# Performance work log

Measured on AMD Instinct MI355X. Metric: run time of the kernel, lower is better.

Reference implementation:

```python
import jax, jax.numpy as jnp
import numpy as np

# model hyperparameters (from init_kwargs 'model' mapping)
SIG = 10.0       # kernel length scale
C = 0.0          # energy integration constant
STD = 1.0        # normalization std
M, N_ATOMS = 64, 24
T_ROWS, DESC = 6000, N_ATOMS * (N_ATOMS - 1) // 2  # 276


def setup_inputs() -> dict:
    key = jax.random.key(0)
    k1, k2, k3 = jax.random.split(key, 3)
    # spread atoms out so pairwise distances are O(1..10) Angstrom-like
    Rs = jax.random.normal(k1, (M, N_ATOMS, 3), jnp.float32) * 3.0
    # training descriptors are inverse distances -> positive values in (0,1)
    xs_train = jax.random.uniform(k2, (T_ROWS, DESC), jnp.float32)
    Jx_alphas = jax.random.normal(k3, (T_ROWS, DESC), jnp.float32) * 0.1
    return {"Rs": Rs, "xs_train": xs_train, "Jx_alphas": Jx_alphas}


def reference(Rs, xs_train, Jx_alphas):
    sig = SIG
    q = np.sqrt(5.0) / sig
    m, n = Rs.shape[0], Rs.shape[1]
    i, j = np.tril_indices(n, k=-1)  # lower-triangular atom pairs, P entries

    # pairwise coordinate differences [M, N, N, 3]
    diffs = Rs[:, :, None, :] - Rs[:, None, :, :]
    # inverse pairwise distances over tril pairs -> descriptor xs [M, P]
    d_ij = jnp.linalg.norm(diffs[:, i, j, :], axis=-1)
    xs = 1.0 / d_ij

    # descriptor differences to all (permuted) training points [M, T, P]
    x_diffs = q * xs[:, None, :] - q * xs_train[None, :, :]
    x_dists = jnp.linalg.norm(x_diffs, axis=-1)            # [M, T]
    exp_xs = (5.0 / (3.0 * sig ** 2)) * jnp.exp(-x_dists)  # [M, T]
    dot = jnp.einsum('mtp,tp->mt', x_diffs, Jx_alphas)     # [M, T]
    exp1 = exp_xs * (1.0 + x_dists)                        # [M, T]

    F1 = jnp.einsum('mt,mtp->mp', exp_xs * dot, x_diffs)   # [M, P]
    F2 = exp1 @ Jx_alphas                                  # [M, P]
    Fs_x = (F1 - F2) * xs ** 3                             # [M, P]

    # scatter pair forces back onto the symmetric [N, N] pair grid;
    # diagonal diffs are zero so leaving mult=0 there matches the original
    mult = jnp.zeros((m, n, n), Rs.dtype)
    mult = mult.at[:, i, j].set(Fs_x).at[:, j, i].set(Fs_x)
    Fs = (diffs * mult[..., None]).sum(axis=1) * STD       # [M, N, 3]

    Es = (exp1 * dot).sum(axis=-1) / q * STD + C           # [M]
    return Es, Fs
```

## Files before the change

kernel.cpp:

```cpp
#include <hip/hip_runtime.h>
#include <math.h>

#define MM 64
#define NA 24
#define NP 276
#define NT 6000
#define NTP 6048
#define QC 0.22360679774997896f
#define EXPC 0.01666666666666667f

#define OFF_XST  0
#define OFF_UU   17664
#define OFF_ES   17728
#define OFF_SW   17792
#define OFF_SH   17856
#define OFF_WT   300480
#define OFF_ET   687552
#define ZTOT     282752

__device__ __forceinline__ float f4c(const float4& v, int i) {
  return i == 0 ? v.x : i == 1 ? v.y : i == 2 ? v.z : v.w;
}

__global__ __launch_bounds__(256) void k_pre(const float* __restrict__ Rs,
                                             float* __restrict__ ws) {
  const int tid = threadIdx.x;
  for (int z = blockIdx.x * 256 + tid; z < ZTOT; z += gridDim.x * 256)
    ws[OFF_ES + z] = 0.f;
  for (int z = blockIdx.x * 256 + tid; z < 6144; z += gridDim.x * 256) {
    if (z < 3072) ws[OFF_WT + 384000 + z] = 0.f;
    else          ws[OFF_ET + 384000 + (z - 3072)] = 0.f;
  }
  if (blockIdx.x < MM) {
    const int m = blockIdx.x;
    __shared__ float sR[NA * 3];
    __shared__ float sAcc[4];
    if (tid < NA * 3) sR[tid] = Rs[m * NA * 3 + tid];
    __syncthreads();
    float acc = 0.f;
    for (int p = tid; p < NP; p += 256) {
      int i = (int)((1.0f + sqrtf(1.0f + 8.0f * (float)p)) * 0.5f);
      while (i * (i - 1) / 2 > p) i--;
      while ((i + 1) * i / 2 <= p) i++;
      int j = p - i * (i - 1) / 2;
      float dx = sR[i * 3 + 0] - sR[j * 3 + 0];
      float dy = sR[i * 3 + 1] - sR[j * 3 + 1];
      float dz = sR[i * 3 + 2] - sR[j * 3 + 2];
      float u = 1.0f / sqrtf(dx * dx + dy * dy + dz * dz);
      ws[OFF_XST + p * 64 + m] = u;
      acc += u * u;
    }
    for (int off = 32; off; off >>= 1) acc += __shfl_down(acc, off);
    if ((tid & 63) == 0) sAcc[tid >> 6] = acc;
    __syncthreads();
    if (tid == 0) ws[OFF_UU + m] = sAcc[0] + sAcc[1] + sAcc[2] + sAcc[3];
  }
}

#define G1_BS 280
#define G1_AS 36
__global__ __launch_bounds__(256, 2) void k_g1(const float* __restrict__ xt,
                                               const float* __restrict__ Ja,
                                               float* __restrict__ ws) {
  __shared__ __align__(16) float2 Bs[16][G1_BS];
  __shared__ __align__(16) float As[NP][G1_AS];
  __shared__ float sVV[16], sC1[16];
  __shared__ float sEsW[4][32], sSwW[4][32];
  const int tid = threadIdx.x;
  const int t0 = blockIdx.x * 16;
  const int m0 = blockIdx.y * 32;

  for (int idx = tid; idx < 16 * 69; idx += 256) {
    const int row = idx / 69;
    const int kq = (idx - row * 69) * 4;
    const float4 v = *(const float4*)(xt + (size_t)(t0 + row) * NP + kq);
    const float4 j = *(const float4*)(Ja + (size_t)(t0 + row) * NP + kq);
    *(float4*)&Bs[row][kq]     = make_float4(v.x, j.x, v.y, j.y);
    *(float4*)&Bs[row][kq + 2] = make_float4(v.z, j.z, v.w, j.w);
  }
  for (int idx = tid; idx < NP * 8; idx += 256) {
    const int p = idx >> 3;
    const int mq = (idx & 7) * 4;
    *(float4*)&As[p][mq] = *(const float4*)(ws + OFF_XST + p * 64 + m0 + mq);
  }
  const int r = tid & 15;
  const int c = tid >> 4;
  const float2 uu2 = *(const float2*)(ws + OFF_UU + m0 + 2 * r);
  __syncthreads();

  {
    const int tl = tid >> 4;
    const int l16 = tid & 15;
    float a = 0.f, b = 0.f;
    for (int k = l16; k < NP; k += 16) {
      const float2 x = Bs[tl][k];
      a = fmaf(x.x, x.x, a);
      b = fmaf(x.x, x.y, b);
    }
#pragma unroll
    for (int off = 8; off; off >>= 1) {
      a += __shfl_down(a, off, 16);
      b += __shfl_down(b, off, 16);
    }
    if (l16 == 0) { sVV[tl] = a; sC1[tl] = b; }
  }
  __syncthreads();

  float av0 = 0.f, av1 = 0.f, aj0 = 0.f, aj1 = 0.f;
#pragma unroll 4
  for (int kk = 0; kk < NP; kk += 2) {
    const float4 b  = *(const float4*)&Bs[c][kk];
    const float2 a0 = *(const float2*)&As[kk][2 * r];
    const float2 a1 = *(const float2*)&As[kk + 1][2 * r];
    av0 = fmaf(a0.x, b.x, av0); aj0 = fmaf(a0.x, b.y, aj0);
    av1 = fmaf(a0.y, b.x, av1); aj1 = fmaf(a0.y, b.y, aj1);
    av0 = fmaf(a1.x, b.z, av0); aj0 = fmaf(a1.x, b.w, aj0);
    av1 = fmaf(a1.y, b.z, av1); aj1 = fmaf(a1.y, b.w, aj1);
  }

  const float vvt = sVV[c];
  const float c1t = sC1[c];
  float es2[2], sw2[2], wv[2], ev[2];
#pragma unroll
  for (int i = 0; i < 2; i++) {
    const float g1v = i ? av1 : av0;
    const float g2v = i ? aj1 : aj0;
    const float uum = i ? uu2.y : uu2.x;
    float d2 = fmaxf(uum - 2.f * g1v + vvt, 0.f);
    float xd = QC * sqrtf(d2);
    float dv = QC * (g2v - c1t);
    float ex = EXPC * __expf(-xd);
    float e1v = ex * (1.f + xd);
    float w_ = ex * dv;
    wv[i] = w_; ev[i] = e1v;
    es2[i] = e1v * dv;
    sw2[i] = w_;
  }
  const int t = t0 + c;
  *(float2*)(ws + OFF_WT + (size_t)t * 64 + m0 + 2 * r) = make_float2(wv[0], wv[1]);
  *(float2*)(ws + OFF_ET + (size_t)t * 64 + m0 + 2 * r) = make_float2(ev[0], ev[1]);

#pragma unroll
  for (int i = 0; i < 2; i++) {
    es2[i] += __shfl_down(es2[i], 32); es2[i] += __shfl_down(es2[i], 16);
    sw2[i] += __shfl_down(sw2[i], 32); sw2[i] += __shfl_down(sw2[i], 16);
  }
  const int w = tid >> 6;
  if ((tid & 63) < 16) {
    sEsW[w][2 * r + 0] = es2[0]; sEsW[w][2 * r + 1] = es2[1];
    sSwW[w][2 * r + 0] = sw2[0]; sSwW[w][2 * r + 1] = sw2[1];
  }
  __syncthreads();
  if (tid < 32) {
    const float es = sEsW[0][tid] + sEsW[1][tid] + sEsW[2][tid] + sEsW[3][tid];
    const float sw = sSwW[0][tid] + sSwW[1][tid] + sSwW[2][tid] + sSwW[3][tid];
    atomicAdd(ws + OFF_ES + m0 + tid, es);
    atomicAdd(ws + OFF_SW + m0 + tid, sw);
  }
}

#define G2_KC 96
#define G2_AS 68
#define G2_BS 18
__global__ __launch_bounds__(256, 2) void k_g2(const float* __restrict__ xt,
                                               const float* __restrict__ Ja,
                                               float* __restrict__ ws) {
  __shared__ __align__(16) float Aw[G2_KC][G2_AS];
  __shared__ __align__(16) float Ae[G2_KC][G2_AS];
  __shared__ __align__(16) float2 Bvj[G2_KC][G2_BS];
  const int tid = threadIdx.x;
  const int p0 = blockIdx.x * 16;
  const int k0 = blockIdx.y * G2_KC;
  const int validp = (NP - p0 < 16) ? (NP - p0) : 16;

  for (int idx = tid; idx < G2_KC * 16; idx += 256) {
    const int k = idx >> 4;
    const int mq = (idx & 15) * 4;
    *(float4*)&Aw[k][mq] = *(const float4*)(ws + OFF_WT + (size_t)(k0 + k) * 64 + mq);
    *(float4*)&Ae[k][mq] = *(const float4*)(ws + OFF_ET + (size_t)(k0 + k) * 64 + mq);
  }
  for (int idx = tid; idx < G2_KC * 4; idx += 256) {
    const int k = idx >> 2;
    const int pq = (idx & 3) * 4;
    const int t = k0 + k;
    float4 v = make_float4(0.f, 0.f, 0.f, 0.f), j = v;
    if (pq < validp && t < NT) {
      v = *(const float4*)(xt + (size_t)t * NP + p0 + pq);
      j = *(const float4*)(Ja + (size_t)t * NP + p0 + pq);
    }
    *(float4*)&Bvj[k][pq]     = make_float4(v.x, j.x, v.y, j.y);
    *(float4*)&Bvj[k][pq + 2] = make_float4(v.z, j.z, v.w, j.w);
  }
  __syncthreads();

  const int r = tid & 31;
  const int c = tid >> 5;
  float f1[2][2] = {{0.f, 0.f}, {0.f, 0.f}};
  float f2[2][2] = {{0.f, 0.f}, {0.f, 0.f}};
#pragma unroll 4
  for (int k = 0; k < G2_KC; k++) {
    const float2 aw = *(const float2*)&Aw[k][2 * r];
    const float2 ae = *(const float2*)&Ae[k][2 * r];
    const float4 b  = *(const float4*)&Bvj[k][2 * c];
    f1[0][0] = fmaf(aw.x, b.x, f1[0][0]); f1[0][1] = fmaf(aw.x, b.z, f1[0][1]);
    f1[1][0] = fmaf(aw.y, b.x, f1[1][0]); f1[1][1] = fmaf(aw.y, b.z, f1[1][1]);
    f2[0][0] = fmaf(ae.x, b.y, f2[0][0]); f2[0][1] = fmaf(ae.x, b.w, f2[0][1]);
    f2[1][0] = fmaf(ae.y, b.y, f2[1][0]); f2[1][1] = fmaf(ae.y, b.w, f2[1][1]);
  }

  const int sh = blockIdx.y & 7;
  float* b1 = ws + OFF_SH + (size_t)(sh * 2 + 0) * NP * 64;
  float* b2 = ws + OFF_SH + (size_t)(sh * 2 + 1) * NP * 64;
#pragma unroll
  for (int j = 0; j < 2; j++) {
    const int pl = 2 * c + j;
    if (pl < validp) {
      const int p = p0 + pl;
#pragma unroll
      for (int i = 0; i < 2; i++) {
        atomicAdd(b1 + (size_t)p * 64 + 2 * r + i, f1[i][j]);
        atomicAdd(b2 + (size_t)p * 64 + 2 * r + i, f2[i][j]);
      }
    }
  }
}

__global__ __launch_bounds__(320) void k_final(const float* __restrict__ Rs,
                                               const float* __restrict__ ws,
                                               float* __restrict__ out) {
  const int m = blockIdx.x;
  const int tid = threadIdx.x;
  __shared__ float fx[NP];
  __shared__ float sR[NA * 3];
  if (tid < NA * 3) sR[tid] = Rs[m * NA * 3 + tid];
  const float sw = ws[OFF_SW + m];
  for (int p = tid; p < NP; p += 320) {
    float f1p = 0.f, f2 = 0.f;
#pragma unroll
    for (int s = 0; s < 8; s++) {
      f1p += ws[OFF_SH + ((size_t)(s * 2 + 0) * NP + p) * 64 + m];
      f2  += ws[OFF_SH + ((size_t)(s * 2 + 1) * NP + p) * 64 + m];
    }
    const float u = ws[OFF_XST + p * 64 + m];
    const float F1 = QC * (u * sw - f1p);
    fx[p] = (F1 - f2) * u * u * u;
  }
  __syncthreads();
  if (tid == 0) out[m] = ws[OFF_ES + m] / QC;
  if (tid < NA * 3) {
    const int a = tid / 3, cc = tid % 3;
    const float ra = sR[a * 3 + cc];
    float acc = 0.f;
    for (int b = 0; b < NA; b++) {
      if (b == a) continue;
      const int i = a > b ? a : b, j = a > b ? b : a;
      const int p = i * (i - 1) / 2 + j;
      acc += (sR[b * 3 + cc] - ra) * fx[p];
    }
    out[MM + m * NA * 3 + tid] = acc;
  }
}

extern "C" void kernel_launch(void* const* d_in, const int* in_sizes, int n_in,
                              void* d_out, int out_size, void* d_ws, size_t ws_size,
                              hipStream_t stream) {
  const float* Rs = (const float*)d_in[0];
  const float* xt = (const float*)d_in[1];
  const float* Ja = (const float*)d_in[2];
  float* out = (float*)d_out;
  float* ws = (float*)d_ws;

  k_pre<<<256, 256, 0, stream>>>(Rs, ws);
  k_g1<<<dim3(375, 2), 256, 0, stream>>>(xt, Ja, ws);
  k_g2<<<dim3(18, 63), 256, 0, stream>>>(xt, Ja, ws);
  k_final<<<MM, 320, 0, stream>>>(Rs, ws, out);
}
```

Baseline: 136.2 us.

## Use split-K register tiling with shared-memory reduction in both GEMM kernels

Result: slower. 151.3 us (+11.1%).

```diff
diff --git a/kernel.cpp b/kernel.cpp
--- a/kernel.cpp
+++ b/kernel.cpp
@@ -57,18 +57,21 @@
   }
 }
 
-#define G1_BS 280
-#define G1_AS 36
+#define G1_BS 278
 __global__ __launch_bounds__(256, 2) void k_g1(const float* __restrict__ xt,
                                                const float* __restrict__ Ja,
                                                float* __restrict__ ws) {
   __shared__ __align__(16) float2 Bs[16][G1_BS];
-  __shared__ __align__(16) float As[NP][G1_AS];
+  __shared__ __align__(16) float As[NP][36];
   __shared__ float sVV[16], sC1[16];
-  __shared__ float sEsW[4][32], sSwW[4][32];
+  __shared__ __align__(16) float sRed[4][64][4];
   const int tid = threadIdx.x;
   const int t0 = blockIdx.x * 16;
   const int m0 = blockIdx.y * 32;
+  const int lane = tid & 63;
+  const int ks = tid >> 6;
+  const int mg = lane & 7;
+  const int tg = lane >> 3;
 
   for (int idx = tid; idx < 16 * 69; idx += 256) {
     const int row = idx / 69;
@@ -83,9 +86,7 @@
     const int mq = (idx & 7) * 4;
     *(float4*)&As[p][mq] = *(const float4*)(ws + OFF_XST + p * 64 + m0 + mq);
   }
-  const int r = tid & 15;
-  const int c = tid >> 4;
-  const float2 uu2 = *(const float2*)(ws + OFF_UU + m0 + 2 * r);
+  const float4 uu4 = *(const float4*)(ws + OFF_UU + m0 + mg * 4);
   __syncthreads();
 
   {
@@ -106,72 +107,109 @@
   }
   __syncthreads();
 
-  float av0 = 0.f, av1 = 0.f, aj0 = 0.f, aj1 = 0.f;
-#pragma unroll 4
-  for (int kk = 0; kk < NP; kk += 2) {
-    const float4 b  = *(const float4*)&Bs[c][kk];
-    const float2 a0 = *(const float2*)&As[kk][2 * r];
-    const float2 a1 = *(const float2*)&As[kk + 1][2 * r];
-    av0 = fmaf(a0.x, b.x, av0); aj0 = fmaf(a0.x, b.y, aj0);
-    av1 = fmaf(a0.y, b.x, av1); aj1 = fmaf(a0.y, b.y, aj1);
-    av0 = fmaf(a1.x, b.z, av0); aj0 = fmaf(a1.x, b.w, aj0);
-    av1 = fmaf(a1.y, b.z, av1); aj1 = fmaf(a1.y, b.w, aj1);
-  }
-
-  const float vvt = sVV[c];
-  const float c1t = sC1[c];
-  float es2[2], sw2[2], wv[2], ev[2];
-#pragma unroll
-  for (int i = 0; i < 2; i++) {
-    const float g1v = i ? av1 : av0;
-    const float g2v = i ? aj1 : aj0;
-    const float uum = i ? uu2.y : uu2.x;
-    float d2 = fmaxf(uum - 2.f * g1v + vvt, 0.f);
-    float xd = QC * sqrtf(d2);
-    float dv = QC * (g2v - c1t);
-    float ex = EXPC * __expf(-xd);
-    float e1v = ex * (1.f + xd);
-    float w_ = ex * dv;
-    wv[i] = w_; ev[i] = e1v;
-    es2[i] = e1v * dv;
-    sw2[i] = w_;
-  }
-  const int t = t0 + c;
-  *(float2*)(ws + OFF_WT + (size_t)t * 64 + m0 + 2 * r) = make_float2(wv[0], wv[1]);
-  *(float2*)(ws + OFF_ET + (size_t)t * 64 + m0 + 2 * r) = make_float2(ev[0], ev[1]);
-
-#pragma unroll
-  for (int i = 0; i < 2; i++) {
-    es2[i] += __shfl_down(es2[i], 32); es2[i] += __shfl_down(es2[i], 16);
-    sw2[i] += __shfl_down(sw2[i], 32); sw2[i] += __shfl_down(sw2[i], 16);
-  }
-  const int w = tid >> 6;
-  if ((tid & 63) < 16) {
-    sEsW[w][2 * r + 0] = es2[0]; sEsW[w][2 * r + 1] = es2[1];
-    sSwW[w][2 * r + 0] = sw2[0]; sSwW[w][2 * r + 1] = sw2[1];
-  }
-  __syncthreads();
-  if (tid < 32) {
-    const float es = sEsW[0][tid] + sEsW[1][tid] + sEsW[2][tid] + sEsW[3][tid];
-    const float sw = sSwW[0][tid] + sSwW[1][tid] + sSwW[2][tid] + sSwW[3][tid];
-    atomicAdd(ws + OFF_ES + m0 + tid, es);
-    atomicAdd(ws + OFF_SW + m0 + tid, sw);
+  float accv[2][4] = {{0.f,0.f,0.f,0.f},{0.f,0.f,0.f,0.f}};
+  float accj[2][4] = {{0.f,0.f,0.f,0.f},{0.f,0.f,0.f,0.f}};
+  const int kbeg = 70 * ks;
+  const int kend = (ks == 3) ? NP : kbeg + 70;
+#pragma unroll 5
+  for (int k = kbeg; k < kend; k += 2) {
+    const float4 bA = *(const float4*)&Bs[2 * tg][k];
+    const float4 bB = *(const float4*)&Bs[2 * tg + 1][k];
+    const float4 a0 = *(const float4*)&As[k][mg * 4];
+    const float4 a1 = *(const float4*)&As[k + 1][mg * 4];
+#pragma unroll
+    for (int i = 0; i < 4; i++) {
+      const float x0 = f4c(a0, i), x1 = f4c(a1, i);
+      accv[0][i] = fmaf(x0, bA.x, accv[0][i]); accj[0][i] = fmaf(x0, bA.y, accj[0][i]);
+      accv[0][i] = fmaf(x1, bA.z, accv[0][i]); accj[0][i] = fmaf(x1, bA.w, accj[0][i]);
+      accv[1][i] = fmaf(x0, bB.x, accv[1][i]); accj[1][i] = fmaf(x0, bB.y, accj[1][i]);
+      accv[1][i] = fmaf(x1, bB.z, accv[1][i]); accj[1][i] = fmaf(x1, bB.w, accj[1][i]);
+    }
+  }
+
+#pragma unroll
+  for (int ps = 0; ps < 4; ps++) {
+    __syncthreads();
+    float4 v;
+    if (ps == 0) v = make_float4(accv[0][0], accv[0][1], accv[0][2], accv[0][3]);
+    else if (ps == 1) v = make_float4(accv[1][0], accv[1][1], accv[1][2], accv[1][3]);
+    else if (ps == 2) v = make_float4(accj[0][0], accj[0][1], accj[0][2], accj[0][3]);
+    else v = make_float4(accj[1][0], accj[1][1], accj[1][2], accj[1][3]);
+    *(float4*)&sRed[ks][lane][0] = v;
+    __syncthreads();
+    if (ks == 0) {
+      const float4 s0 = *(const float4*)&sRed[0][lane][0];
+      const float4 s1 = *(const float4*)&sRed[1][lane][0];
+      const float4 s2 = *(const float4*)&sRed[2][lane][0];
+      const float4 s3 = *(const float4*)&sRed[3][lane][0];
+      const float4 s = make_float4(s0.x + s1.x + s2.x + s3.x, s0.y + s1.y + s2.y + s3.y,
+                                   s0.z + s1.z + s2.z + s3.z, s0.w + s1.w + s2.w + s3.w);
+      if (ps == 0)      { accv[0][0]=s.x; accv[0][1]=s.y; accv[0][2]=s.z; accv[0][3]=s.w; }
+      else if (ps == 1) { accv[1][0]=s.x; accv[1][1]=s.y; accv[1][2]=s.z; accv[1][3]=s.w; }
+      else if (ps == 2) { accj[0][0]=s.x; accj[0][1]=s.y; accj[0][2]=s.z; accj[0][3]=s.w; }
+      else              { accj[1][0]=s.x; accj[1][1]=s.y; accj[1][2]=s.z; accj[1][3]=s.w; }
+    }
+  }
+
+  if (ks == 0) {
+    float es4[4] = {0.f,0.f,0.f,0.f}, sw4[4] = {0.f,0.f,0.f,0.f};
+#pragma unroll
+    for (int tt = 0; tt < 2; tt++) {
+      const int t = t0 + tg * 2 + tt;
+      const float vvt = sVV[tg * 2 + tt];
+      const float c1t = sC1[tg * 2 + tt];
+      float wq[4], eq[4];
+#pragma unroll
+      for (int i = 0; i < 4; i++) {
+        float d2 = fmaxf(f4c(uu4, i) - 2.f * accv[tt][i] + vvt, 0.f);
+        float xd = QC * sqrtf(d2);
+        float dv = QC * (accj[tt][i] - c1t);
+        float ex = EXPC * __expf(-xd);
+        float e1v = ex * (1.f + xd);
+        float w_ = ex * dv;
+        wq[i] = w_; eq[i] = e1v;
+        es4[i] += e1v * dv;
+        sw4[i] += w_;
+      }
+      *(float4*)(ws + OFF_WT + (size_t)t * 64 + m0 + mg * 4) =
+          make_float4(wq[0], wq[1], wq[2], wq[3]);
+      *(float4*)(ws + OFF_ET + (size_t)t * 64 + m0 + mg * 4) =
+          make_float4(eq[0], eq[1], eq[2], eq[3]);
+    }
+#pragma unroll
+    for (int off = 8; off <= 32; off <<= 1) {
+#pragma unroll
+      for (int i = 0; i < 4; i++) {
+        es4[i] += __shfl_down(es4[i], off);
+        sw4[i] += __shfl_down(sw4[i], off);
+      }
+    }
+    if (tg == 0) {
+#pragma unroll
+      for (int i = 0; i < 4; i++) {
+        atomicAdd(ws + OFF_ES + m0 + mg * 4 + i, es4[i]);
+        atomicAdd(ws + OFF_SW + m0 + mg * 4 + i, sw4[i]);
+      }
+    }
   }
 }
 
 #define G2_KC 96
-#define G2_AS 68
-#define G2_BS 18
 __global__ __launch_bounds__(256, 2) void k_g2(const float* __restrict__ xt,
                                                const float* __restrict__ Ja,
                                                float* __restrict__ ws) {
-  __shared__ __align__(16) float Aw[G2_KC][G2_AS];
-  __shared__ __align__(16) float Ae[G2_KC][G2_AS];
-  __shared__ __align__(16) float2 Bvj[G2_KC][G2_BS];
+  __shared__ __align__(16) float Aw[G2_KC][68];
+  __shared__ __align__(16) float Ae[G2_KC][68];
+  __shared__ __align__(16) float2 Bvj[G2_KC][18];
+  __shared__ __align__(16) float sRed[4][64][8];
   const int tid = threadIdx.x;
   const int p0 = blockIdx.x * 16;
   const int k0 = blockIdx.y * G2_KC;
   const int validp = (NP - p0 < 16) ? (NP - p0) : 16;
+  const int lane = tid & 63;
+  const int ks = tid >> 6;
+  const int mg = lane & 15;
+  const int pg = lane >> 4;
 
   for (int idx = tid; idx < G2_KC * 16; idx += 256) {
     const int k = idx >> 4;
@@ -193,34 +231,72 @@
   }
   __syncthreads();
 
-  const int r = tid & 31;
-  const int c = tid >> 5;
-  float f1[2][2] = {{0.f, 0.f}, {0.f, 0.f}};
-  float f2[2][2] = {{0.f, 0.f}, {0.f, 0.f}};
+  float f1[4][4] = {{0}}, f2[4][4] = {{0}};
+  const int kb = ks * 24;
 #pragma unroll 4
-  for (int k = 0; k < G2_KC; k++) {
-    const float2 aw = *(const float2*)&Aw[k][2 * r];
-    const float2 ae = *(const float2*)&Ae[k][2 * r];
-    const float4 b  = *(const float4*)&Bvj[k][2 * c];
-    f1[0][0] = fmaf(aw.x, b.x, f1[0][0]); f1[0][1] = fmaf(aw.x, b.z, f1[0][1]);
-    f1[1][0] = fmaf(aw.y, b.x, f1[1][0]); f1[1][1] = fmaf(aw.y, b.z, f1[1][1]);
-    f2[0][0] = fmaf(ae.x, b.y, f2[0][0]); f2[0][1] = fmaf(ae.x, b.w, f2[0][1]);
-    f2[1][0] = fmaf(ae.y, b.y, f2[1][0]); f2[1][1] = fmaf(ae.y, b.w, f2[1][1]);
-  }
-
+  for (int k = kb; k < kb + 24; k++) {
+    const float4 aw = *(const float4*)&Aw[k][mg * 4];
+    const float4 ae = *(const float4*)&Ae[k][mg * 4];
+    const float4 b0 = *(const float4*)&Bvj[k][pg * 4];
+    const float4 b1 = *(const float4*)&Bvj[k][pg * 4 + 2];
+#pragma unroll
+    for (int i = 0; i < 4; i++) {
+      const float w_ = f4c(aw, i), e_ = f4c(ae, i);
+      f1[i][0] = fmaf(w_, b0.x, f1[i][0]); f2[i][0] = fmaf(e_, b0.y, f2[i][0]);
+      f1[i][1] = fmaf(w_, b0.z, f1[i][1]); f2[i][1] = fmaf(e_, b0.w, f2[i][1]);
+      f1[i][2] = fmaf(w_, b1.x, f1[i][2]); f2[i][2] = fmaf(e_, b1.y, f2[i][2]);
+      f1[i][3] = fmaf(w_, b1.z, f1[i][3]); f2[i][3] = fmaf(e_, b1.w, f2[i][3]);
+    }
+  }
+
+#pragma unroll
+  for (int ps = 0; ps < 4; ps++) {
+    const int i0 = (ps & 1) * 2;
+    float (*src)[4] = (ps < 2) ? f1 : f2;
+    __syncthreads();
+    *(float4*)&sRed[ks][lane][0] = make_float4(src[i0][0], src[i0][1], src[i0][2], src[i0][3]);
+    *(float4*)&sRed[ks][lane][4] = make_float4(src[i0+1][0], src[i0+1][1], src[i0+1][2], src[i0+1][3]);
+    __syncthreads();
+    if (ks == 0) {
+#pragma unroll
+      for (int h = 0; h < 2; h++) {
+        const float4 s0 = *(const float4*)&sRed[0][lane][4 * h];
+        const float4 s1 = *(const float4*)&sRed[1][lane][4 * h];
+        const float4 s2 = *(const float4*)&sRed[2][lane][4 * h];
+        const float4 s3 = *(const float4*)&sRed[3][lane][4 * h];
+        src[i0 + h][0] = s0.x + s1.x + s2.x + s3.x;
+        src[i0 + h][1] = s0.y + s1.y + s2.y + s3.y;
+        src[i0 + h][2] = s0.z + s1.z + s2.z + s3.z;
+        src[i0 + h][3] = s0.w + s1.w + s2.w + s3.w;
+      }
+    }
+  }
+
+  float* redP = &sRed[0][0][0];
+  __syncthreads();
+  if (ks == 0) {
+#pragma unroll
+    for (int j = 0; j < 4; j++) {
+      const int pl = pg * 4 + j;
+#pragma unroll
+      for (int i = 0; i < 4; i++) {
+        redP[pl * 64 + mg * 4 + i]        = f1[i][j];
+        redP[(16 + pl) * 64 + mg * 4 + i] = f2[i][j];
+      }
+    }
+  }
+  __syncthreads();
+  const int m = tid & 63;
   const int sh = blockIdx.y & 7;
   float* b1 = ws + OFF_SH + (size_t)(sh * 2 + 0) * NP * 64;
   float* b2 = ws + OFF_SH + (size_t)(sh * 2 + 1) * NP * 64;
 #pragma unroll
-  for (int j = 0; j < 2; j++) {
-    const int pl = 2 * c + j;
+  for (int q = 0; q < 4; q++) {
+    const int pl = (tid >> 6) + q * 4;
     if (pl < validp) {
       const int p = p0 + pl;
-#pragma unroll
-      for (int i = 0; i < 2; i++) {
-        atomicAdd(b1 + (size_t)p * 64 + 2 * r + i, f1[i][j]);
-        atomicAdd(b2 + (size_t)p * 64 + 2 * r + i, f2[i][j]);
-      }
+      atomicAdd(b1 + (size_t)p * 64 + m, redP[pl * 64 + m]);
+      atomicAdd(b2 + (size_t)p * 64 + m, redP[(16 + pl) * 64 + m]);
     }
   }
 }
```

## Fuse descriptor precompute into k_g1, drop atomics for per-block partial sums

Applied to the files above, without the earlier changes.

Result: slower. 150.7 us (+10.6%).

```diff
diff --git a/kernel.cpp b/kernel.cpp
--- a/kernel.cpp
+++ b/kernel.cpp
@@ -9,91 +9,96 @@
 #define QC 0.22360679774997896f
 #define EXPC 0.01666666666666667f
 
-#define OFF_XST  0
-#define OFF_UU   17664
-#define OFF_ES   17728
-#define OFF_SW   17792
-#define OFF_SH   17856
-#define OFF_WT   300480
-#define OFF_ET   687552
-#define ZTOT     282752
+#define OFF_SH   0
+#define OFF_PES  282624
+#define OFF_PSW  306624
+#define OFF_WT   330624
+#define OFF_ET   717696
 
 __device__ __forceinline__ float f4c(const float4& v, int i) {
   return i == 0 ? v.x : i == 1 ? v.y : i == 2 ? v.z : v.w;
 }
 
-__global__ __launch_bounds__(256) void k_pre(const float* __restrict__ Rs,
-                                             float* __restrict__ ws) {
+#define S_BS  0
+#define S_AS  8896
+#define S_VV  18280
+#define S_C1  18296
+#define S_UU  18312
+#define S_UUF 18568
+#define S_ESW 18600
+#define S_SWW 18728
+#define S_TOT 18856
+__global__ __launch_bounds__(256, 2) void k_g1(const float* __restrict__ Rs,
+                                               const float* __restrict__ xt,
+                                               const float* __restrict__ Ja,
+                                               float* __restrict__ ws) {
+  __shared__ __align__(16) float smem[S_TOT];
   const int tid = threadIdx.x;
-  for (int z = blockIdx.x * 256 + tid; z < ZTOT; z += gridDim.x * 256)
-    ws[OFF_ES + z] = 0.f;
-  for (int z = blockIdx.x * 256 + tid; z < 6144; z += gridDim.x * 256) {
-    if (z < 3072) ws[OFF_WT + 384000 + z] = 0.f;
-    else          ws[OFF_ET + 384000 + (z - 3072)] = 0.f;
-  }
-  if (blockIdx.x < MM) {
-    const int m = blockIdx.x;
-    __shared__ float sR[NA * 3];
-    __shared__ float sAcc[4];
-    if (tid < NA * 3) sR[tid] = Rs[m * NA * 3 + tid];
-    __syncthreads();
-    float acc = 0.f;
-    for (int p = tid; p < NP; p += 256) {
+  const int t0 = blockIdx.x * 16;
+  const int m0 = blockIdx.y * 32;
+
+  {
+    const int gid = blockIdx.y * 375 + blockIdx.x;
+    for (int z = gid * 256 + tid; z < 288768; z += 192000) {
+      if (z < 282624)      ws[OFF_SH + z] = 0.f;
+      else if (z < 285696) ws[OFF_WT + 384000 + (z - 282624)] = 0.f;
+      else                 ws[OFF_ET + 384000 + (z - 285696)] = 0.f;
+    }
+  }
+
+  for (int idx = tid; idx < 32 * 72; idx += 256) {
+    const int ml = idx / 72, q = idx - ml * 72;
+    smem[S_BS + ml * 73 + q] = Rs[(size_t)(m0 + ml) * 72 + q];
+  }
+  __syncthreads();
+
+  {
+    const int ml = tid & 31;
+    const float* sR = smem + S_BS + ml * 73;
+    float uup = 0.f;
+    for (int p = tid >> 5; p < NP; p += 8) {
       int i = (int)((1.0f + sqrtf(1.0f + 8.0f * (float)p)) * 0.5f);
       while (i * (i - 1) / 2 > p) i--;
       while ((i + 1) * i / 2 <= p) i++;
-      int j = p - i * (i - 1) / 2;
-      float dx = sR[i * 3 + 0] - sR[j * 3 + 0];
-      float dy = sR[i * 3 + 1] - sR[j * 3 + 1];
-      float dz = sR[i * 3 + 2] - sR[j * 3 + 2];
-      float u = 1.0f / sqrtf(dx * dx + dy * dy + dz * dz);
-      ws[OFF_XST + p * 64 + m] = u;
-      acc += u * u;
-    }
-    for (int off = 32; off; off >>= 1) acc += __shfl_down(acc, off);
-    if ((tid & 63) == 0) sAcc[tid >> 6] = acc;
-    __syncthreads();
-    if (tid == 0) ws[OFF_UU + m] = sAcc[0] + sAcc[1] + sAcc[2] + sAcc[3];
-  }
-}
-
-#define G1_BS 280
-#define G1_AS 36
-__global__ __launch_bounds__(256, 2) void k_g1(const float* __restrict__ xt,
-                                               const float* __restrict__ Ja,
-                                               float* __restrict__ ws) {
-  __shared__ __align__(16) float2 Bs[16][G1_BS];
-  __shared__ __align__(16) float As[NP][G1_AS];
-  __shared__ float sVV[16], sC1[16];
-  __shared__ float sEsW[4][32], sSwW[4][32];
-  const int tid = threadIdx.x;
-  const int t0 = blockIdx.x * 16;
-  const int m0 = blockIdx.y * 32;
-
-  for (int idx = tid; idx < 16 * 69; idx += 256) {
-    const int row = idx / 69;
-    const int kq = (idx - row * 69) * 4;
-    const float4 v = *(const float4*)(xt + (size_t)(t0 + row) * NP + kq);
-    const float4 j = *(const float4*)(Ja + (size_t)(t0 + row) * NP + kq);
-    *(float4*)&Bs[row][kq]     = make_float4(v.x, j.x, v.y, j.y);
-    *(float4*)&Bs[row][kq + 2] = make_float4(v.z, j.z, v.w, j.w);
-  }
-  for (int idx = tid; idx < NP * 8; idx += 256) {
-    const int p = idx >> 3;
-    const int mq = (idx & 7) * 4;
-    *(float4*)&As[p][mq] = *(const float4*)(ws + OFF_XST + p * 64 + m0 + mq);
-  }
-  const int r = tid & 15;
-  const int c = tid >> 4;
-  const float2 uu2 = *(const float2*)(ws + OFF_UU + m0 + 2 * r);
-  __syncthreads();
-
-  {
+      const int j = p - i * (i - 1) / 2;
+      const float dx = sR[i * 3 + 0] - sR[j * 3 + 0];
+      const float dy = sR[i * 3 + 1] - sR[j * 3 + 1];
+      const float dz = sR[i * 3 + 2] - sR[j * 3 + 2];
+      const float u = 1.0f / sqrtf(dx * dx + dy * dy + dz * dz);
+      smem[S_AS + p * 34 + ml] = u;
+      uup = fmaf(u, u, uup);
+    }
+    smem[S_UU + (tid >> 5) * 32 + ml] = uup;
+  }
+  __syncthreads();
+  if (tid < 32) {
+    float s = 0.f;
+#pragma unroll
+    for (int k = 0; k < 8; k++) s += smem[S_UU + k * 32 + tid];
+    smem[S_UUF + tid] = s;
+  }
+  __syncthreads();
+
+  {
+    float2* Bs = (float2*)(smem + S_BS);
+    for (int idx = tid; idx < 16 * 69; idx += 256) {
+      const int row = idx / 69;
+      const int kq = (idx - row * 69) * 4;
+      const float4 v = *(const float4*)(xt + (size_t)(t0 + row) * NP + kq);
+      const float4 j = *(const float4*)(Ja + (size_t)(t0 + row) * NP + kq);
+      *(float4*)&Bs[row * 278 + kq]     = make_float4(v.x, j.x, v.y, j.y);
+      *(float4*)&Bs[row * 278 + kq + 2] = make_float4(v.z, j.z, v.w, j.w);
+    }
+  }
+  __syncthreads();
+
+  {
+    const float2* Bs = (const float2*)(smem + S_BS);
     const int tl = tid >> 4;
     const int l16 = tid & 15;
     float a = 0.f, b = 0.f;
     for (int k = l16; k < NP; k += 16) {
-      const float2 x = Bs[tl][k];
+      const float2 x = Bs[tl * 278 + k];
       a = fmaf(x.x, x.x, a);
       b = fmaf(x.x, x.y, b);
     }
@@ -102,30 +107,37 @@
       a += __shfl_down(a, off, 16);
       b += __shfl_down(b, off, 16);
     }
-    if (l16 == 0) { sVV[tl] = a; sC1[tl] = b; }
-  }
-  __syncthreads();
-
+    if (l16 == 0) { smem[S_VV + tl] = a; smem[S_C1 + tl] = b; }
+  }
+  __syncthreads();
+
+  const int r = tid & 15;
+  const int c = tid >> 4;
   float av0 = 0.f, av1 = 0.f, aj0 = 0.f, aj1 = 0.f;
+  {
+    const float2* Bs = (const float2*)(smem + S_BS);
 #pragma unroll 4
-  for (int kk = 0; kk < NP; kk += 2) {
-    const float4 b  = *(const float4*)&Bs[c][kk];
-    const float2 a0 = *(const float2*)&As[kk][2 * r];
-    const float2 a1 = *(const float2*)&As[kk + 1][2 * r];
-    av0 = fmaf(a0.x, b.x, av0); aj0 = fmaf(a0.x, b.y, aj0);
-    av1 = fmaf(a0.y, b.x, av1); aj1 = fmaf(a0.y, b.y, aj1);
-    av0 = fmaf(a1.x, b.z, av0); aj0 = fmaf(a1.x, b.w, aj0);
-    av1 = fmaf(a1.y, b.z, av1); aj1 = fmaf(a1.y, b.w, aj1);
-  }
-
-  const float vvt = sVV[c];
-  const float c1t = sC1[c];
+    for (int kk = 0; kk < NP; kk += 2) {
+      const float4 b  = *(const float4*)&Bs[c * 278 + kk];
+      const float2 a0 = *(const float2*)&smem[S_AS + kk * 34 + 2 * r];
+      const float2 a1 = *(const float2*)&smem[S_AS + (kk + 1) * 34 + 2 * r];
+      av0 = fmaf(a0.x, b.x, av0); aj0 = fmaf(a0.x, b.y, aj0);
+      av1 = fmaf(a0.y, b.x, av1); aj1 = fmaf(a0.y, b.y, aj1);
+      av0 = fmaf(a1.x, b.z, av0); aj0 = fmaf(a1.x, b.w, aj0);
+      av1 = fmaf(a1.y, b.z, av1); aj1 = fmaf(a1.y, b.w, aj1);
+    }
+  }
+
+  const float vvt = smem[S_VV + c];
+  const float c1t = smem[S_C1 + c];
+  const float uum0 = smem[S_UUF + 2 * r];
+  const float uum1 = smem[S_UUF + 2 * r + 1];
   float es2[2], sw2[2], wv[2], ev[2];
 #pragma unroll
   for (int i = 0; i < 2; i++) {
     const float g1v = i ? av1 : av0;
     const float g2v = i ? aj1 : aj0;
-    const float uum = i ? uu2.y : uu2.x;
+    const float uum = i ? uum1 : uum0;
     float d2 = fmaxf(uum - 2.f * g1v + vvt, 0.f);
     float xd = QC * sqrtf(d2);
     float dv = QC * (g2v - c1t);
@@ -147,27 +159,31 @@
   }
   const int w = tid >> 6;
   if ((tid & 63) < 16) {
-    sEsW[w][2 * r + 0] = es2[0]; sEsW[w][2 * r + 1] = es2[1];
-    sSwW[w][2 * r + 0] = sw2[0]; sSwW[w][2 * r + 1] = sw2[1];
+    smem[S_ESW + w * 32 + 2 * r + 0] = es2[0];
+    smem[S_ESW + w * 32 + 2 * r + 1] = es2[1];
+    smem[S_SWW + w * 32 + 2 * r + 0] = sw2[0];
+    smem[S_SWW + w * 32 + 2 * r + 1] = sw2[1];
   }
   __syncthreads();
   if (tid < 32) {
-    const float es = sEsW[0][tid] + sEsW[1][tid] + sEsW[2][tid] + sEsW[3][tid];
-    const float sw = sSwW[0][tid] + sSwW[1][tid] + sSwW[2][tid] + sSwW[3][tid];
-    atomicAdd(ws + OFF_ES + m0 + tid, es);
-    atomicAdd(ws + OFF_SW + m0 + tid, sw);
+    float es = 0.f, sw = 0.f;
+#pragma unroll
+    for (int k = 0; k < 4; k++) {
+      es += smem[S_ESW + k * 32 + tid];
+      sw += smem[S_SWW + k * 32 + tid];
+    }
+    ws[OFF_PES + (size_t)blockIdx.y * 375 * 32 + blockIdx.x * 32 + tid] = es;
+    ws[OFF_PSW + (size_t)blockIdx.y * 375 * 32 + blockIdx.x * 32 + tid] = sw;
   }
 }
 
 #define G2_KC 96
-#define G2_AS 68
-#define G2_BS 18
 __global__ __launch_bounds__(256, 2) void k_g2(const float* __restrict__ xt,
                                                const float* __restrict__ Ja,
                                                float* __restrict__ ws) {
-  __shared__ __align__(16) float Aw[G2_KC][G2_AS];
-  __shared__ __align__(16) float Ae[G2_KC][G2_AS];
-  __shared__ __align__(16) float2 Bvj[G2_KC][G2_BS];
+  __shared__ __align__(16) float Aw[G2_KC][68];
+  __shared__ __align__(16) float Ae[G2_KC][68];
+  __shared__ __align__(16) float2 Bvj[G2_KC][18];
   const int tid = threadIdx.x;
   const int p0 = blockIdx.x * 16;
   const int k0 = blockIdx.y * G2_KC;
@@ -232,21 +248,54 @@
   const int tid = threadIdx.x;
   __shared__ float fx[NP];
   __shared__ float sR[NA * 3];
-  if (tid < NA * 3) sR[tid] = Rs[m * NA * 3 + tid];
-  const float sw = ws[OFF_SW + m];
-  for (int p = tid; p < NP; p += 320) {
+  __shared__ float sE[5], sW[5], sFin[2];
+  if (tid < NA * 3) sR[tid] = Rs[(size_t)m * 72 + tid];
+
+  {
+    const int half = m >> 5, ml = m & 31;
+    float esp = 0.f, swp = 0.f;
+    for (int b = tid; b < 375; b += 320) {
+      esp += ws[OFF_PES + (size_t)half * 375 * 32 + b * 32 + ml];
+      swp += ws[OFF_PSW + (size_t)half * 375 * 32 + b * 32 + ml];
+    }
+#pragma unroll
+    for (int off = 32; off; off >>= 1) {
+      esp += __shfl_down(esp, off);
+      swp += __shfl_down(swp, off);
+    }
+    if ((tid & 63) == 0) { sE[tid >> 6] = esp; sW[tid >> 6] = swp; }
+  }
+  __syncthreads();
+  if (tid == 0) {
+    float es = 0.f, sw = 0.f;
+#pragma unroll
+    for (int k = 0; k < 5; k++) { es += sE[k]; sw += sW[k]; }
+    sFin[0] = es; sFin[1] = sw;
+  }
+  __syncthreads();
+  const float sw = sFin[1];
+
+  if (tid < NP) {
+    const int p = tid;
+    int i = (int)((1.0f + sqrtf(1.0f + 8.0f * (float)p)) * 0.5f);
+    while (i * (i - 1) / 2 > p) i--;
+    while ((i + 1) * i / 2 <= p) i++;
+    const int j = p - i * (i - 1) / 2;
+    const float dx = sR[i * 3 + 0] - sR[j * 3 + 0];
+    const float dy = sR[i * 3 + 1] - sR[j * 3 + 1];
+    const float dz = sR[i * 3 + 2] - sR[j * 3 + 2];
+    const float u = 1.0f / sqrtf(dx * dx + dy * dy + dz * dz);
     float f1p = 0.f, f2 = 0.f;
 #pragma unroll
     for (int s = 0; s < 8; s++) {
       f1p += ws[OFF_SH + ((size_t)(s * 2 + 0) * NP + p) * 64 + m];
       f2  += ws[OFF_SH + ((size_t)(s * 2 + 1) * NP + p) * 64 + m];
     }
-    const float u = ws[OFF_XST + p * 64 + m];
     const float F1 = QC * (u * sw - f1p);
     fx[p] = (F1 - f2) * u * u * u;
   }
   __syncthreads();
-  if (tid == 0) out[m] = ws[OFF_ES + m] / QC;
+  if (tid == 0) out[m] = sFin[0] / QC;
   if (tid < NA * 3) {
     const int a = tid / 3, cc = tid % 3;
     const float ra = sR[a * 3 + cc];
@@ -257,7 +306,7 @@
       const int p = i * (i - 1) / 2 + j;
       acc += (sR[b * 3 + cc] - ra) * fx[p];
     }
-    out[MM + m * NA * 3 + tid] = acc;
+    out[MM + (size_t)m * NA * 3 + tid] = acc;
   }
 }
 
@@ -270,8 +319,7 @@
   float* out = (float*)d_out;
   float* ws = (float*)d_ws;
 
-  k_pre<<<256, 256, 0, stream>>>(Rs, ws);
-  k_g1<<<dim3(375, 2), 256, 0, stream>>>(xt, Ja, ws);
+  k_g1<<<dim3(375, 2), 256, 0, stream>>>(Rs, xt, Ja, ws);
   k_g2<<<dim3(18, 63), 256, 0, stream>>>(xt, Ja, ws);
   k_final<<<MM, 320, 0, stream>>>(Rs, ws, out);
 }
```
